# Kernel tuning notes

Hardware: AMD Instinct MI355X
Metric: run time of the kernel (lower is better)

The kernel has to match this reference:

```python
import jax, jax.numpy as jnp
import numpy as np

P, F, H, OUT = 2, 64, 2, 2   # passes, inputLayerSize, heads, outputLayerSize
N, E = 50000, 400000
D_JUMP = (P + 1) * F          # 192, JumpingKnowledge 'cat' output
D_FC = D_JUMP + 1             # 193, after concat with problemType
D_HID = D_FC // 2             # 96


def setup_inputs() -> dict:
    key = jax.random.key(0)
    ks = jax.random.split(key, 20)
    s = 1.0 / np.sqrt(F)
    return {
        'x': jax.random.normal(ks[0], (N, F), dtype=jnp.float32),
        'edge_index': jax.random.randint(ks[1], (2, E), 0, N, dtype=jnp.int32),
        'edge_attr': jax.random.normal(ks[2], (E, 1), dtype=jnp.float32),
        'problemType': jax.random.normal(ks[3], (1,), dtype=jnp.float32),
        'batch': jnp.zeros((N,), dtype=jnp.int32),
        # stacked GATv2Conv params over the P layers
        'lin_l_w': jax.random.normal(ks[4], (P, F, H * F)) * s,
        'lin_l_b': jnp.zeros((P, H * F), jnp.float32),
        'lin_r_w': jax.random.normal(ks[5], (P, F, H * F)) * s,
        'lin_r_b': jnp.zeros((P, H * F), jnp.float32),
        'lin_edge_w': jax.random.normal(ks[6], (P, 1, H * F)) * s,
        'att': jax.random.normal(ks[7], (P, H, F)) * s,
        'gat_bias': jnp.zeros((P, F), jnp.float32),
        # GlobalAttention gate_nn: Linear(D_JUMP, 1) + LeakyReLU
        'gate_w': jax.random.normal(ks[8], (D_JUMP, 1)) / np.sqrt(D_JUMP),
        'gate_b': jnp.zeros((1,), jnp.float32),
        'fc1_w': jax.random.normal(ks[9], (D_FC, D_HID)) / np.sqrt(D_FC),
        'fc1_b': jnp.zeros((D_HID,), jnp.float32),
        'fc2_w': jax.random.normal(ks[10], (D_HID, D_HID)) / np.sqrt(D_HID),
        'fc2_b': jnp.zeros((D_HID,), jnp.float32),
        'fcl_w': jax.random.normal(ks[11], (D_HID, OUT)) / np.sqrt(D_HID),
        'fcl_b': jnp.zeros((OUT,), jnp.float32),
    }


def _gatv2_layer(x, src, dst, edge_attr, Wl, bl, Wr, br, We, att, bias):
    """GATv2Conv with concat=False (mean over heads), edge_dim=1."""
    n = x.shape[0]
    xl = (x @ Wl + bl).reshape(n, H, F)          # source transform
    xr = (x @ Wr + br).reshape(n, H, F)          # target transform
    ef = (edge_attr @ We).reshape(-1, H, F)      # edge transform (no bias)
    m = xl[src] + xr[dst] + ef                   # [E,H,F]
    m = jax.nn.leaky_relu(m, 0.2)
    logits = jnp.einsum('ehf,hf->eh', m, att)    # [E,H]
    # segment softmax over destination node
    lmax = jax.ops.segment_max(logits, dst, num_segments=n)
    a = jnp.exp(logits - lmax[dst])
    denom = jax.ops.segment_sum(a, dst, num_segments=n)
    alpha = a / denom[dst]                       # [E,H]
    msg = xl[src] * alpha[:, :, None]            # [E,H,F]
    out = jax.ops.segment_sum(msg, dst, num_segments=n)  # [N,H,F]
    return out.mean(axis=1) + bias               # concat=False -> head mean


def reference(x, edge_index, edge_attr, problemType, batch,
              lin_l_w, lin_l_b, lin_r_w, lin_r_b, lin_edge_w, att, gat_bias,
              gate_w, gate_b, fc1_w, fc1_b, fc2_w, fc2_b, fcl_w, fcl_b):
    src, dst = edge_index[0], edge_index[1]
    xs = [x]
    h = x
    for p in range(P):
        h = _gatv2_layer(h, src, dst, edge_attr,
                         lin_l_w[p], lin_l_b[p], lin_r_w[p], lin_r_b[p],
                         lin_edge_w[p], att[p], gat_bias[p])
        h = jax.nn.leaky_relu(h, 0.01)
        xs.append(h)
    xj = jnp.concatenate(xs, axis=1)             # JumpingKnowledge 'cat' -> [N, D_JUMP]
    # GlobalAttention pooling (single graph: batch is all zeros)
    gate = jax.nn.leaky_relu(xj @ gate_w + gate_b, 0.01)  # [N,1]
    a = jax.nn.softmax(gate, axis=0)
    pooled = jnp.sum(a * xj, axis=0, keepdims=True)       # [1, D_JUMP]
    z = jnp.concatenate([pooled.reshape(1, -1), problemType[:, None]], axis=1)  # [1, D_FC]
    z = jax.nn.leaky_relu(z @ fc1_w + fc1_b, 0.01)
    z = jax.nn.leaky_relu(z @ fc2_w + fc2_b, 0.01)
    return z @ fcl_w + fcl_b                     # [1, OUT]
```

## Files before the change

### kernel.cpp

```cpp
#include <hip/hip_runtime.h>

#define NN 50000
#define NE 400000
#define FD 64
#define NH 2
#define HF 128
#define SCAN_NB ((NN + 255) / 256)
#define POOL_BLOCKS 512
#define NTA 64
#define GG_BLOCKS 2048

__device__ __forceinline__ float lrelu(float x, float s) { return fmaxf(x, x * s); }

__device__ __forceinline__ unsigned short f2bf(float f) {
    unsigned u = __float_as_uint(f);
    return (unsigned short)((u + 0x7FFFu + ((u >> 16) & 1u)) >> 16);
}
__device__ __forceinline__ float2 bf2f(unsigned u) {
    return make_float2(__uint_as_float(u << 16), __uint_as_float(u & 0xFFFF0000u));
}
__device__ __forceinline__ float4 bfx4(unsigned lo, unsigned hi) {
    const float2 a = bf2f(lo), b = bf2f(hi);
    return make_float4(a.x, a.y, b.x, b.y);
}

__global__ void count_deg(const int* __restrict__ ei, int* __restrict__ deg) {
    const int t = blockIdx.x * blockDim.x + threadIdx.x;
    if (t < NE) atomicAdd(&deg[ei[NE + t]], 1);
}

__global__ void block_sums(const int* __restrict__ deg, int* __restrict__ bsum) {
    __shared__ int s[4];
    const int t = threadIdx.x;
    const int i = blockIdx.x * 256 + t;
    int v = (i < NN) ? deg[i] : 0;
#pragma unroll
    for (int o = 32; o; o >>= 1) v += __shfl_xor(v, o);
    if ((t & 63) == 0) s[t >> 6] = v;
    __syncthreads();
    if (t == 0) bsum[blockIdx.x] = s[0] + s[1] + s[2] + s[3];
}

__global__ void write_base(const int* __restrict__ deg, const int* __restrict__ bsum,
                           int* __restrict__ base, int2* __restrict__ rng,
                           int* __restrict__ cursor) {
    __shared__ int s[256];
    __shared__ int soff[4];
    const int t = threadIdx.x;
    const int bid = blockIdx.x;
    int v0 = (t < bid && t < SCAN_NB) ? bsum[t] : 0;
#pragma unroll
    for (int o = 32; o; o >>= 1) v0 += __shfl_xor(v0, o);
    if ((t & 63) == 0) soff[t >> 6] = v0;
    const int i = bid * 256 + t;
    const int v = (i < NN) ? deg[i] : 0;
    s[t] = v;
    __syncthreads();
    const int off = soff[0] + soff[1] + soff[2] + soff[3];
    for (int o = 1; o < 256; o <<= 1) {
        int u = (t >= o) ? s[t - o] : 0;
        __syncthreads();
        s[t] += u;
        __syncthreads();
    }
    if (i < NN) {
        const int b = off + s[t] - v;
        base[i] = b;
        rng[i] = make_int2(b, b + v);
        cursor[i] = 0;
    }
}

__global__ void scatter_edges(const int* __restrict__ ei, const float* __restrict__ ea,
                              const int* __restrict__ base, int* __restrict__ cursor,
                              int2* __restrict__ csr) {
    const int t = blockIdx.x * blockDim.x + threadIdx.x;
    if (t >= NE) return;
    const int d = ei[NE + t];
    const int p = atomicAdd(&cursor[d], 1);
    const int i = base[d] + p;
    csr[i] = make_int2(ei[t], __float_as_int(ea[t]));
}

__global__ __launch_bounds__(256) void node_transform(
    const float* __restrict__ hin,
    const float* __restrict__ Wl, const float* __restrict__ bl,
    const float* __restrict__ Wr, const float* __restrict__ br,
    unsigned short* __restrict__ xlb, unsigned short* __restrict__ xrb) {
    __shared__ float sA[FD][68];
    const int t = threadIdx.x;
    const int n0 = blockIdx.x * NTA;
    for (int idx = t; idx < NTA * 16; idx += 256) {
        const int n = idx & 63;
        const int kq = (idx >> 6) << 2;
        const int ni = n0 + n;
        const float4 v = (ni < NN) ? *(const float4*)(hin + (size_t)ni * FD + kq)
                                   : make_float4(0.f, 0.f, 0.f, 0.f);
        sA[kq][n] = v.x; sA[kq + 1][n] = v.y;
        sA[kq + 2][n] = v.z; sA[kq + 3][n] = v.w;
    }
    __syncthreads();
    const int q = t & 63;
    const int g = t >> 6;
    const int c0 = q << 2;
    const bool isR = c0 >= 128;
    const int cc = isR ? c0 - 128 : c0;
    const float* __restrict__ W = isR ? Wr : Wl;
    const float4 bv = isR ? *(const float4*)(br + cc) : *(const float4*)(bl + cc);
    unsigned short* __restrict__ dst = isR ? xrb : xlb;
    float acc[16][4];
#pragma unroll
    for (int i = 0; i < 16; ++i) {
        acc[i][0] = bv.x; acc[i][1] = bv.y; acc[i][2] = bv.z; acc[i][3] = bv.w;
    }
    const int nb = g << 4;
#pragma unroll 4
    for (int k = 0; k < FD; ++k) {
        const float4 w = *(const float4*)(W + k * HF + cc);
        const float4 a0 = *(const float4*)(&sA[k][nb]);
        const float4 a1 = *(const float4*)(&sA[k][nb + 4]);
        const float4 a2 = *(const float4*)(&sA[k][nb + 8]);
        const float4 a3 = *(const float4*)(&sA[k][nb + 12]);
        const float av[16] = {a0.x, a0.y, a0.z, a0.w, a1.x, a1.y, a1.z, a1.w,
                              a2.x, a2.y, a2.z, a2.w, a3.x, a3.y, a3.z, a3.w};
#pragma unroll
        for (int i = 0; i < 16; ++i) {
            acc[i][0] = fmaf(av[i], w.x, acc[i][0]);
            acc[i][1] = fmaf(av[i], w.y, acc[i][1]);
            acc[i][2] = fmaf(av[i], w.z, acc[i][2]);
            acc[i][3] = fmaf(av[i], w.w, acc[i][3]);
        }
    }
    const int xoff = (cc < 64) ? (cc << 1) : (((cc - 64) << 1) + 4);
#pragma unroll
    for (int i = 0; i < 16; ++i) {
        const int n = n0 + nb + i;
        if (n >= NN) continue;
        uint2 pk;
        pk.x = (unsigned)f2bf(acc[i][0]) | ((unsigned)f2bf(acc[i][1]) << 16);
        pk.y = (unsigned)f2bf(acc[i][2]) | ((unsigned)f2bf(acc[i][3]) << 16);
        *(uint2*)(dst + (size_t)n * HF + xoff) = pk;
    }
}

__device__ __forceinline__ void gat_edge(
    bool valid, int lane, float eav, uint4 L,
    const float4& we0, const float4& we1, const float4& aw0, const float4& aw1,
    const float4& xr0, const float4& xr1,
    float4& a0, float4& a1, float& d0, float& d1) {
    const float4 xls0 = bfx4(L.x, L.y);
    const float4 xls1 = bfx4(L.z, L.w);
    float p0, p1, t;
    t = lrelu(fmaf(eav, we0.x, xls0.x + xr0.x), 0.2f); p0 = t * aw0.x;
    t = lrelu(fmaf(eav, we0.y, xls0.y + xr0.y), 0.2f); p0 = fmaf(t, aw0.y, p0);
    t = lrelu(fmaf(eav, we0.z, xls0.z + xr0.z), 0.2f); p0 = fmaf(t, aw0.z, p0);
    t = lrelu(fmaf(eav, we0.w, xls0.w + xr0.w), 0.2f); p0 = fmaf(t, aw0.w, p0);
    t = lrelu(fmaf(eav, we1.x, xls1.x + xr1.x), 0.2f); p1 = t * aw1.x;
    t = lrelu(fmaf(eav, we1.y, xls1.y + xr1.y), 0.2f); p1 = fmaf(t, aw1.y, p1);
    t = lrelu(fmaf(eav, we1.z, xls1.z + xr1.z), 0.2f); p1 = fmaf(t, aw1.z, p1);
    t = lrelu(fmaf(eav, we1.w, xls1.w + xr1.w), 0.2f); p1 = fmaf(t, aw1.w, p1);
    const bool hi = (lane & 8) != 0;
    float send = hi ? p0 : p1;
    float got = __shfl_xor(send, 8);
    float q = hi ? (p1 + got) : (p0 + got);
    q += __shfl_xor(q, 4);
    q += __shfl_xor(q, 2);
    q += __shfl_xor(q, 1);
    const float oth = __shfl_xor(q, 8);
    const float s0 = hi ? oth : q;
    const float s1 = hi ? q : oth;
    const float w0 = valid ? __expf(s0) : 0.f;
    const float w1 = valid ? __expf(s1) : 0.f;
    a0.x = fmaf(w0, xls0.x, a0.x);
    a0.y = fmaf(w0, xls0.y, a0.y);
    a0.z = fmaf(w0, xls0.z, a0.z);
    a0.w = fmaf(w0, xls0.w, a0.w);
    d0 += w0;
    a1.x = fmaf(w1, xls1.x, a1.x);
    a1.y = fmaf(w1, xls1.y, a1.y);
    a1.z = fmaf(w1, xls1.z, a1.z);
    a1.w = fmaf(w1, xls1.w, a1.w);
    d1 += w1;
}

__global__ __launch_bounds__(256) void gat_gather(
    const int2* __restrict__ rng, const int2* __restrict__ csr,
    const unsigned short* __restrict__ xlb, const unsigned short* __restrict__ xrb,
    const float* __restrict__ We, const float* __restrict__ att,
    const float* __restrict__ bias, float* __restrict__ hout) {
    const int t = threadIdx.x;
    const int lane = t & 63;
    const int slot = lane >> 4;
    const int fo = (lane & 15) << 2;
    const float4 we0 = *(const float4*)(We + fo);
    const float4 we1 = *(const float4*)(We + 64 + fo);
    const float4 aw0 = *(const float4*)(att + fo);
    const float4 aw1 = *(const float4*)(att + 64 + fo);
    const float4 bv = *(const float4*)(bias + fo);
    const int stride = (GG_BLOCKS * 256) >> 6;
    int wid = (blockIdx.x * 256 + t) >> 6;
    int2 r = (wid < NN) ? rng[wid] : make_int2(0, 0);

    while (wid < NN) {
        const int nxt = wid + stride;
        const int2 rn = (nxt < NN) ? rng[nxt] : make_int2(0, 0);
        const uint4 xrp = *(const uint4*)(xrb + (size_t)wid * HF + (fo << 1));
        const float4 xr0 = bfx4(xrp.x, xrp.y);
        const float4 xr1 = bfx4(xrp.z, xrp.w);
        const int e0 = r.x, e1 = r.y;
        float d0 = 0.f, d1 = 0.f;
        float4 a0 = {0.f, 0.f, 0.f, 0.f}, a1 = {0.f, 0.f, 0.f, 0.f};
        int eb = e0;
        for (; eb + 8 <= e1; eb += 8) {
            const int2 seA = csr[eb + slot];
            const int2 seB = csr[eb + 4 + slot];
            const uint4 LA = *(const uint4*)(xlb + (size_t)seA.x * HF + (fo << 1));
            const uint4 LB = *(const uint4*)(xlb + (size_t)seB.x * HF + (fo << 1));
            gat_edge(true, lane, __int_as_float(seA.y), LA, we0, we1, aw0, aw1,
                     xr0, xr1, a0, a1, d0, d1);
            gat_edge(true, lane, __int_as_float(seB.y), LB, we0, we1, aw0, aw1,
                     xr0, xr1, a0, a1, d0, d1);
        }
        if (eb < e1) {
            const int myA = eb + slot, myB = eb + 4 + slot;
            const bool vA = myA < e1, vB = myB < e1;
            const int2 seA = csr[vA ? myA : e0];
            const int2 seB = csr[vB ? myB : e0];
            const uint4 LA = *(const uint4*)(xlb + (size_t)seA.x * HF + (fo << 1));
            const uint4 LB = *(const uint4*)(xlb + (size_t)seB.x * HF + (fo << 1));
            gat_edge(vA, lane, __int_as_float(seA.y), LA, we0, we1, aw0, aw1,
                     xr0, xr1, a0, a1, d0, d1);
            gat_edge(vB, lane, __int_as_float(seB.y), LB, we0, we1, aw0, aw1,
                     xr0, xr1, a0, a1, d0, d1);
        }
#pragma unroll
        for (int o = 16; o <= 32; o <<= 1) {
            d0 += __shfl_xor(d0, o);
            d1 += __shfl_xor(d1, o);
            a0.x += __shfl_xor(a0.x, o); a0.y += __shfl_xor(a0.y, o);
            a0.z += __shfl_xor(a0.z, o); a0.w += __shfl_xor(a0.w, o);
            a1.x += __shfl_xor(a1.x, o); a1.y += __shfl_xor(a1.y, o);
            a1.z += __shfl_xor(a1.z, o); a1.w += __shfl_xor(a1.w, o);
        }
        if (slot == 0) {
            const float i0 = d0 > 0.f ? 1.f / d0 : 0.f;
            const float i1 = d1 > 0.f ? 1.f / d1 : 0.f;
            float4 rr;
            rr.x = lrelu(fmaf(0.5f, fmaf(a0.x, i0, a1.x * i1), bv.x), 0.01f);
            rr.y = lrelu(fmaf(0.5f, fmaf(a0.y, i0, a1.y * i1), bv.y), 0.01f);
            rr.z = lrelu(fmaf(0.5f, fmaf(a0.z, i0, a1.z * i1), bv.z), 0.01f);
            rr.w = lrelu(fmaf(0.5f, fmaf(a0.w, i0, a1.w * i1), bv.w), 0.01f);
            *(float4*)(hout + (size_t)wid * FD + fo) = rr;
        }
        wid = nxt;
        r = rn;
    }
}

__global__ void pool_kernel(const float* __restrict__ x, const float* __restrict__ h1,
                            const float* __restrict__ h2, const float* __restrict__ gw,
                            const float* __restrict__ gb, float* __restrict__ part) {
    __shared__ float sp[193];
    const int t = threadIdx.x;
    if (t < 193) sp[t] = 0.f;
    __syncthreads();
    const int lane = t & 63;
    const int wid = (blockIdx.x * blockDim.x + t) >> 6;
    const int nw = (POOL_BLOCKS * 256) >> 6;
    const float w0 = gw[lane], w1 = gw[64 + lane], w2 = gw[128 + lane];
    const float gbv = gb[0];
    float p0 = 0.f, p1 = 0.f, p2 = 0.f, es = 0.f;
    for (int n = wid; n < NN; n += nw) {
        const size_t b = (size_t)n * FD + lane;
        const float xv = x[b], h1v = h1[b], h2v = h2[b];
        float v = xv * w0 + h1v * w1 + h2v * w2;
#pragma unroll
        for (int o = 32; o; o >>= 1) v += __shfl_xor(v, o);
        const float e = __expf(lrelu(v + gbv, 0.01f));
        p0 = fmaf(e, xv, p0);
        p1 = fmaf(e, h1v, p1);
        p2 = fmaf(e, h2v, p2);
        es += e;
    }
    atomicAdd(&sp[lane], p0);
    atomicAdd(&sp[64 + lane], p1);
    atomicAdd(&sp[128 + lane], p2);
    if (lane == 0) atomicAdd(&sp[192], es);
    __syncthreads();
    if (t < 193) part[blockIdx.x * 196 + t] = sp[t];
}

__global__ void mlp_kernel(const float* __restrict__ part, const float* __restrict__ pt,
                           const float* __restrict__ f1w, const float* __restrict__ f1b,
                           const float* __restrict__ f2w, const float* __restrict__ f2b,
                           const float* __restrict__ flw, const float* __restrict__ flb,
                           float* __restrict__ out) {
    __shared__ float z[193], z1[96], z2[96];
    const int t = threadIdx.x;
    if (t < 193) {
        float s = 0.f;
        for (int b = 0; b < POOL_BLOCKS; ++b) s += part[b * 196 + t];
        z[t] = s;
    }
    __syncthreads();
    const float inv = 1.f / z[192];
    __syncthreads();
    for (int i = t; i < 192; i += 256) z[i] *= inv;
    if (t == 0) z[192] = pt[0];
    __syncthreads();
    if (t < 96) {
        float a = f1b[t];
        for (int k = 0; k < 193; ++k) a = fmaf(z[k], f1w[k * 96 + t], a);
        z1[t] = lrelu(a, 0.01f);
    }
    __syncthreads();
    if (t < 96) {
        float a = f2b[t];
        for (int k = 0; k < 96; ++k) a = fmaf(z1[k], f2w[k * 96 + t], a);
        z2[t] = lrelu(a, 0.01f);
    }
    __syncthreads();
    if (t < 2) {
        float a = flb[t];
        for (int k = 0; k < 96; ++k) a = fmaf(z2[k], flw[k * 2 + t], a);
        out[t] = a;
    }
}

extern "C" void kernel_launch(void* const* d_in, const int* in_sizes, int n_in,
                              void* d_out, int out_size, void* d_ws, size_t ws_size,
                              hipStream_t stream) {
    (void)in_sizes; (void)n_in; (void)out_size; (void)ws_size;
    const float* x    = (const float*)d_in[0];
    const int*   ei   = (const int*)d_in[1];
    const float* ea   = (const float*)d_in[2];
    const float* pt   = (const float*)d_in[3];
    const float* llw  = (const float*)d_in[5];
    const float* llb  = (const float*)d_in[6];
    const float* lrw  = (const float*)d_in[7];
    const float* lrb  = (const float*)d_in[8];
    const float* lew  = (const float*)d_in[9];
    const float* attw = (const float*)d_in[10];
    const float* gbias= (const float*)d_in[11];
    const float* gw   = (const float*)d_in[12];
    const float* gb   = (const float*)d_in[13];
    const float* f1w  = (const float*)d_in[14];
    const float* f1b  = (const float*)d_in[15];
    const float* f2w  = (const float*)d_in[16];
    const float* f2b  = (const float*)d_in[17];
    const float* flw  = (const float*)d_in[18];
    const float* flb  = (const float*)d_in[19];
    float* out = (float*)d_out;

    char* w = (char*)d_ws;
    unsigned short* xlb = (unsigned short*)w; w += (size_t)NN * HF * 2;
    unsigned short* xrb = (unsigned short*)w; w += (size_t)NN * HF * 2;
    float* h1 = (float*)w;         w += (size_t)NN * FD * 4;
    float* h2 = (float*)w;         w += (size_t)NN * FD * 4;
    int2* csr = (int2*)w;          w += (size_t)NE * 8;
    int* deg = (int*)w;            w += (size_t)NN * 4;
    int* csr_base = (int*)w;       w += (size_t)(NN + 1) * 4;
    int2* rng = (int2*)w;          w += (size_t)NN * 8;
    int* cursor = (int*)w;         w += (size_t)NN * 4;
    int* bsum = (int*)w;           w += (size_t)SCAN_NB * 4;
    float* part = (float*)w;       w += (size_t)POOL_BLOCKS * 196 * 4;

    hipMemsetAsync(deg, 0, (size_t)NN * 4, stream);
    count_deg<<<(NE + 255) / 256, 256, 0, stream>>>(ei, deg);
    block_sums<<<SCAN_NB, 256, 0, stream>>>(deg, bsum);
    write_base<<<SCAN_NB, 256, 0, stream>>>(deg, bsum, csr_base, rng, cursor);
    scatter_edges<<<(NE + 255) / 256, 256, 0, stream>>>(ei, ea, csr_base, cursor, csr);

    for (int p = 0; p < 2; ++p) {
        const float* hin = (p == 0) ? x : h1;
        float* hout = (p == 0) ? h1 : h2;
        node_transform<<<(NN + NTA - 1) / NTA, 256, 0, stream>>>(
            hin, llw + (size_t)p * FD * HF, llb + (size_t)p * HF,
            lrw + (size_t)p * FD * HF, lrb + (size_t)p * HF, xlb, xrb);
        gat_gather<<<GG_BLOCKS, 256, 0, stream>>>(
            rng, csr, xlb, xrb,
            lew + (size_t)p * HF, attw + (size_t)p * HF,
            gbias + (size_t)p * FD, hout);
    }

    pool_kernel<<<POOL_BLOCKS, 256, 0, stream>>>(x, h1, h2, gw, gb, part);
    mlp_kernel<<<1, 256, 0, stream>>>(part, pt, f1w, f1b, f2w, f2b, flw, flb, out);
}
```

Baseline: 237.2 us.

## Fuse attention pooling into second GAT gather and reuse atomic ranks for CSR

Count_deg stores each edge's atomicAdd return value as its rank within its destination. Scatter_edges then places edges without a second atomic pass or cursor reset. The second gat_gather computes the gate and softmax-weighted partial sums inline instead of writing h2 and launching a separate pool kernel, saving the h2 write and read traffic. In exchange it adds many shared-memory atomics per node and quadruples the number of partials the single-block MLP must reduce.

```diff
diff --git a/kernel.cpp b/kernel.cpp
--- a/kernel.cpp
+++ b/kernel.cpp
@@ -6,7 +6,6 @@
 #define NH 2
 #define HF 128
 #define SCAN_NB ((NN + 255) / 256)
-#define POOL_BLOCKS 512
 #define NTA 64
 #define GG_BLOCKS 2048
 
@@ -24,9 +23,10 @@
     return make_float4(a.x, a.y, b.x, b.y);
 }
 
-__global__ void count_deg(const int* __restrict__ ei, int* __restrict__ deg) {
+__global__ void count_deg(const int* __restrict__ ei, int* __restrict__ deg,
+                          int* __restrict__ rank) {
     const int t = blockIdx.x * blockDim.x + threadIdx.x;
-    if (t < NE) atomicAdd(&deg[ei[NE + t]], 1);
+    if (t < NE) rank[t] = atomicAdd(&deg[ei[NE + t]], 1);
 }
 
 __global__ void block_sums(const int* __restrict__ deg, int* __restrict__ bsum) {
@@ -42,8 +42,7 @@
 }
 
 __global__ void write_base(const int* __restrict__ deg, const int* __restrict__ bsum,
-                           int* __restrict__ base, int2* __restrict__ rng,
-                           int* __restrict__ cursor) {
+                           int* __restrict__ base, int2* __restrict__ rng) {
     __shared__ int s[256];
     __shared__ int soff[4];
     const int t = threadIdx.x;
@@ -67,19 +66,16 @@
         const int b = off + s[t] - v;
         base[i] = b;
         rng[i] = make_int2(b, b + v);
-        cursor[i] = 0;
     }
 }
 
 __global__ void scatter_edges(const int* __restrict__ ei, const float* __restrict__ ea,
-                              const int* __restrict__ base, int* __restrict__ cursor,
+                              const int* __restrict__ base, const int* __restrict__ rank,
                               int2* __restrict__ csr) {
     const int t = blockIdx.x * blockDim.x + threadIdx.x;
     if (t >= NE) return;
     const int d = ei[NE + t];
-    const int p = atomicAdd(&cursor[d], 1);
-    const int i = base[d] + p;
-    csr[i] = make_int2(ei[t], __float_as_int(ea[t]));
+    csr[base[d] + rank[t]] = make_int2(ei[t], __float_as_int(ea[t]));
 }
 
 __global__ __launch_bounds__(256) void node_transform(
@@ -183,12 +179,21 @@
     d1 += w1;
 }
 
+template <bool POOL>
 __global__ __launch_bounds__(256) void gat_gather(
     const int2* __restrict__ rng, const int2* __restrict__ csr,
     const unsigned short* __restrict__ xlb, const unsigned short* __restrict__ xrb,
     const float* __restrict__ We, const float* __restrict__ att,
-    const float* __restrict__ bias, float* __restrict__ hout) {
-    const int t = threadIdx.x;
+    const float* __restrict__ bias, float* __restrict__ hout,
+    const float* __restrict__ x, const float* __restrict__ h1,
+    const float* __restrict__ gw, const float* __restrict__ gb,
+    float* __restrict__ part) {
+    __shared__ float sp[193];
+    const int t = threadIdx.x;
+    if (POOL) {
+        if (t < 193) sp[t] = 0.f;
+        __syncthreads();
+    }
     const int lane = t & 63;
     const int slot = lane >> 4;
     const int fo = (lane & 15) << 2;
@@ -197,6 +202,7 @@
     const float4 aw0 = *(const float4*)(att + fo);
     const float4 aw1 = *(const float4*)(att + 64 + fo);
     const float4 bv = *(const float4*)(bias + fo);
+    const float gbv = POOL ? gb[0] : 0.f;
     const int stride = (GG_BLOCKS * 256) >> 6;
     int wid = (blockIdx.x * 256 + t) >> 6;
     int2 r = (wid < NN) ? rng[wid] : make_int2(0, 0);
@@ -250,44 +256,46 @@
             rr.y = lrelu(fmaf(0.5f, fmaf(a0.y, i0, a1.y * i1), bv.y), 0.01f);
             rr.z = lrelu(fmaf(0.5f, fmaf(a0.z, i0, a1.z * i1), bv.z), 0.01f);
             rr.w = lrelu(fmaf(0.5f, fmaf(a0.w, i0, a1.w * i1), bv.w), 0.01f);
-            *(float4*)(hout + (size_t)wid * FD + fo) = rr;
+            if (POOL) {
+                const float4 xq = *(const float4*)(x + (size_t)wid * FD + fo);
+                const float4 hq = *(const float4*)(h1 + (size_t)wid * FD + fo);
+                const float4 g0 = *(const float4*)(gw + fo);
+                const float4 g1 = *(const float4*)(gw + 64 + fo);
+                const float4 g2 = *(const float4*)(gw + 128 + fo);
+                float v = xq.x * g0.x + xq.y * g0.y + xq.z * g0.z + xq.w * g0.w;
+                v = fmaf(hq.x, g1.x, v); v = fmaf(hq.y, g1.y, v);
+                v = fmaf(hq.z, g1.z, v); v = fmaf(hq.w, g1.w, v);
+                v = fmaf(rr.x, g2.x, v); v = fmaf(rr.y, g2.y, v);
+                v = fmaf(rr.z, g2.z, v); v = fmaf(rr.w, g2.w, v);
+                v += __shfl_xor(v, 1);
+                v += __shfl_xor(v, 2);
+                v += __shfl_xor(v, 4);
+                v += __shfl_xor(v, 8);
+                const float e = __expf(lrelu(v + gbv, 0.01f));
+                atomicAdd(&sp[fo],       e * xq.x);
+                atomicAdd(&sp[fo + 1],   e * xq.y);
+                atomicAdd(&sp[fo + 2],   e * xq.z);
+                atomicAdd(&sp[fo + 3],   e * xq.w);
+                atomicAdd(&sp[64 + fo],     e * hq.x);
+                atomicAdd(&sp[64 + fo + 1], e * hq.y);
+                atomicAdd(&sp[64 + fo + 2], e * hq.z);
+                atomicAdd(&sp[64 + fo + 3], e * hq.w);
+                atomicAdd(&sp[128 + fo],     e * rr.x);
+                atomicAdd(&sp[128 + fo + 1], e * rr.y);
+                atomicAdd(&sp[128 + fo + 2], e * rr.z);
+                atomicAdd(&sp[128 + fo + 3], e * rr.w);
+                if (fo == 0) atomicAdd(&sp[192], e);
+            } else {
+                *(float4*)(hout + (size_t)wid * FD + fo) = rr;
+            }
         }
         wid = nxt;
         r = rn;
     }
-}
-
-__global__ void pool_kernel(const float* __restrict__ x, const float* __restrict__ h1,
-                            const float* __restrict__ h2, const float* __restrict__ gw,
-                            const float* __restrict__ gb, float* __restrict__ part) {
-    __shared__ float sp[193];
-    const int t = threadIdx.x;
-    if (t < 193) sp[t] = 0.f;
-    __syncthreads();
-    const int lane = t & 63;
-    const int wid = (blockIdx.x * blockDim.x + t) >> 6;
-    const int nw = (POOL_BLOCKS * 256) >> 6;
-    const float w0 = gw[lane], w1 = gw[64 + lane], w2 = gw[128 + lane];
-    const float gbv = gb[0];
-    float p0 = 0.f, p1 = 0.f, p2 = 0.f, es = 0.f;
-    for (int n = wid; n < NN; n += nw) {
-        const size_t b = (size_t)n * FD + lane;
-        const float xv = x[b], h1v = h1[b], h2v = h2[b];
-        float v = xv * w0 + h1v * w1 + h2v * w2;
-#pragma unroll
-        for (int o = 32; o; o >>= 1) v += __shfl_xor(v, o);
-        const float e = __expf(lrelu(v + gbv, 0.01f));
-        p0 = fmaf(e, xv, p0);
-        p1 = fmaf(e, h1v, p1);
-        p2 = fmaf(e, h2v, p2);
-        es += e;
-    }
-    atomicAdd(&sp[lane], p0);
-    atomicAdd(&sp[64 + lane], p1);
-    atomicAdd(&sp[128 + lane], p2);
-    if (lane == 0) atomicAdd(&sp[192], es);
-    __syncthreads();
-    if (t < 193) part[blockIdx.x * 196 + t] = sp[t];
+    if (POOL) {
+        __syncthreads();
+        if (t < 193) part[blockIdx.x * 196 + t] = sp[t];
+    }
 }
 
 __global__ void mlp_kernel(const float* __restrict__ part, const float* __restrict__ pt,
@@ -299,7 +307,8 @@
     const int t = threadIdx.x;
     if (t < 193) {
         float s = 0.f;
-        for (int b = 0; b < POOL_BLOCKS; ++b) s += part[b * 196 + t];
+#pragma unroll 8
+        for (int b = 0; b < GG_BLOCKS; ++b) s += part[b * 196 + t];
         z[t] = s;
     }
     __syncthreads();
@@ -356,33 +365,32 @@
     unsigned short* xlb = (unsigned short*)w; w += (size_t)NN * HF * 2;
     unsigned short* xrb = (unsigned short*)w; w += (size_t)NN * HF * 2;
     float* h1 = (float*)w;         w += (size_t)NN * FD * 4;
-    float* h2 = (float*)w;         w += (size_t)NN * FD * 4;
     int2* csr = (int2*)w;          w += (size_t)NE * 8;
+    int* rank = (int*)w;           w += (size_t)NE * 4;
     int* deg = (int*)w;            w += (size_t)NN * 4;
     int* csr_base = (int*)w;       w += (size_t)(NN + 1) * 4;
     int2* rng = (int2*)w;          w += (size_t)NN * 8;
-    int* cursor = (int*)w;         w += (size_t)NN * 4;
     int* bsum = (int*)w;           w += (size_t)SCAN_NB * 4;
-    float* part = (float*)w;       w += (size_t)POOL_BLOCKS * 196 * 4;
+    float* part = (float*)w;       w += (size_t)GG_BLOCKS * 196 * 4;
 
     hipMemsetAsync(deg, 0, (size_t)NN * 4, stream);
-    count_deg<<<(NE + 255) / 256, 256, 0, stream>>>(ei, deg);
+    count_deg<<<(NE + 255) / 256, 256, 0, stream>>>(ei, deg, rank);
     block_sums<<<SCAN_NB, 256, 0, stream>>>(deg, bsum);
-    write_base<<<SCAN_NB, 256, 0, stream>>>(deg, bsum, csr_base, rng, cursor);
-    scatter_edges<<<(NE + 255) / 256, 256, 0, stream>>>(ei, ea, csr_base, cursor, csr);
-
-    for (int p = 0; p < 2; ++p) {
-        const float* hin = (p == 0) ? x : h1;
-        float* hout = (p == 0) ? h1 : h2;
-        node_transform<<<(NN + NTA - 1) / NTA, 256, 0, stream>>>(
-            hin, llw + (size_t)p * FD * HF, llb + (size_t)p * HF,
-            lrw + (size_t)p * FD * HF, lrb + (size_t)p * HF, xlb, xrb);
-        gat_gather<<<GG_BLOCKS, 256, 0, stream>>>(
-            rng, csr, xlb, xrb,
-            lew + (size_t)p * HF, attw + (size_t)p * HF,
-            gbias + (size_t)p * FD, hout);
-    }
-
-    pool_kernel<<<POOL_BLOCKS, 256, 0, stream>>>(x, h1, h2, gw, gb, part);
+    write_base<<<SCAN_NB, 256, 0, stream>>>(deg, bsum, csr_base, rng);
+    scatter_edges<<<(NE + 255) / 256, 256, 0, stream>>>(ei, ea, csr_base, rank, csr);
+
+    node_transform<<<(NN + NTA - 1) / NTA, 256, 0, stream>>>(
+        x, llw, llb, lrw, lrb, xlb, xrb);
+    gat_gather<false><<<GG_BLOCKS, 256, 0, stream>>>(
+        rng, csr, xlb, xrb, lew, attw, gbias, h1,
+        nullptr, nullptr, nullptr, nullptr, nullptr);
+
+    node_transform<<<(NN + NTA - 1) / NTA, 256, 0, stream>>>(
+        h1, llw + (size_t)FD * HF, llb + HF,
+        lrw + (size_t)FD * HF, lrb + HF, xlb, xrb);
+    gat_gather<true><<<GG_BLOCKS, 256, 0, stream>>>(
+        rng, csr, xlb, xrb, lew + HF, attw + HF, gbias + FD, nullptr,
+        x, h1, gw, gb, part);
+
     mlp_kernel<<<1, 256, 0, stream>>>(part, pt, f1w, f1b, f2w, f2b, flw, flb, out);
 }
```

Measured after the change: 319.9 us. 34.9% more time.
